# Kernel optimization log

Measured on AMD Instinct MI355X. Metric: run time of the kernel, lower is better.

## Reference

```python
import jax, jax.numpy as jnp
import numpy as np

L, D = 1024, 256
NDIR, NL = 6, 2
H, P, N, K = 8, 64, 32, 4          # nheads, headdim, d_state, d_conv
DI = 2 * D                          # d_inner = expand * d_model
DIN = 2 * DI + 2 * N + H            # in_proj output width (z, xBC, dt)
CONV_DIM = DI + 2 * N               # channels going through depthwise conv
ORDERS = [(0, 1, 2), (0, 2, 1), (1, 0, 2), (1, 2, 0), (2, 0, 1), (2, 1, 0)]  # XYT,XTY,YXT,YTX,TXY,TYX


def setup_inputs() -> dict:
    ks = jax.random.split(jax.random.key(0), 12)
    s = 0.02
    f32 = jnp.float32
    return {
        "vectors": jax.random.normal(ks[0], (L, D), f32),
        "event_coords": jax.random.randint(ks[1], (L, 4), 0, 64, jnp.int32),
        "ln_g": jnp.ones((NDIR, NL, D), f32),
        "ln_b": jnp.zeros((NDIR, NL, D), f32),
        "Win": jax.random.normal(ks[2], (NDIR, NL, D, DIN), f32) * s,
        "conv_w": jax.random.normal(ks[3], (NDIR, NL, CONV_DIM, K), f32) * s,
        "conv_b": jnp.zeros((NDIR, NL, CONV_DIM), f32),
        "dt_bias": jax.random.normal(ks[4], (NDIR, NL, H), f32) * 0.5,
        "A_log": jnp.log(jax.random.uniform(ks[5], (NDIR, NL, H), f32, 1.0, 16.0)),
        "Dp": jnp.ones((NDIR, NL, H), f32),
        "rms_g": jnp.ones((NDIR, NL, DI), f32),
        "Wout": jax.random.normal(ks[6], (NDIR, NL, DI, D), f32) * s,
        "fuse_ln_g": jnp.ones((NDIR * D,), f32),
        "fuse_ln_b": jnp.zeros((NDIR * D,), f32),
        "fuse_W": jax.random.normal(ks[7], (NDIR * D, D), f32) * s,
        "fuse_b": jnp.zeros((D,), f32),
    }


def _layernorm(x, g, b, eps=1e-5):
    mu = jnp.mean(x, -1, keepdims=True)
    var = jnp.mean((x - mu) ** 2, -1, keepdims=True)
    return (x - mu) * jax.lax.rsqrt(var + eps) * g + b


def _causal_dwconv(x, w, b):
    # x: [Bt,L,C]; w: [C,K]. Torch depthwise conv1d with padding K-1, truncated to L.
    k = w.shape[1]
    Lx = x.shape[1]
    xp = jnp.pad(x, ((0, 0), (k - 1, 0), (0, 0)))
    return sum(xp[:, j:j + Lx, :] * w[:, j] for j in range(k)) + b


def _mamba2(x, Win, conv_w, conv_b, dt_bias, A_log, Dp, rms_g, Wout):
    # x: [Bt,L,D] -> [Bt,L,D]. Mamba2 with ngroups=1, rmsnorm gating, no proj biases.
    Bt, Lx, _ = x.shape
    zxbcdt = x @ Win
    z = zxbcdt[..., :DI]
    xBC = zxbcdt[..., DI:DI + CONV_DIM]
    dt = jax.nn.softplus(zxbcdt[..., -H:] + dt_bias)              # [Bt,L,H]
    xBC = jax.nn.silu(_causal_dwconv(xBC, conv_w, conv_b))
    xs = xBC[..., :DI].reshape(Bt, Lx, H, P)                      # [Bt,L,H,P]
    Bm = xBC[..., DI:DI + N]                                      # [Bt,L,N]
    Cm = xBC[..., DI + N:]                                        # [Bt,L,N]
    dA = jnp.exp(dt * (-jnp.exp(A_log)))                          # [Bt,L,H]
    dBx = jnp.einsum('blh,bln,blhp->blhpn', dt, Bm, xs)

    def step(h, inp):
        dA_t, dBx_t, C_t = inp
        h = dA_t[:, :, None, None] * h + dBx_t                    # [Bt,H,P,N]
        return h, jnp.einsum('bhpn,bn->bhp', h, C_t)

    h0 = jnp.zeros((Bt, H, P, N), x.dtype)
    _, ys = jax.lax.scan(step, h0, (dA.transpose(1, 0, 2),
                                    dBx.transpose(1, 0, 2, 3, 4),
                                    Cm.transpose(1, 0, 2)))
    y = ys.transpose(1, 0, 2, 3) + Dp[:, None] * xs               # [Bt,L,H,P]
    u = y.reshape(Bt, Lx, DI) * jax.nn.silu(z)                    # gated RMSNorm
    u = u * jax.lax.rsqrt(jnp.mean(u * u, -1, keepdims=True) + 1e-5) * rms_g
    return u @ Wout


def _forward(vectors, event_coords, ln_g, ln_b, Win, conv_w, conv_b, dt_bias,
             A_log, Dp, rms_g, Wout, fuse_ln_g, fuse_ln_b, fuse_W, fuse_b):
    v = vectors[None]                                             # [1,L,D]
    outs = []
    for i, axes in enumerate(ORDERS):
        idx = jnp.lexsort(tuple(event_coords[:, a] for a in reversed(axes)))
        x = v[:, idx, :]
        for l in range(NL):
            x = x + _mamba2(_layernorm(x, ln_g[i, l], ln_b[i, l]),
                            Win[i, l], conv_w[i, l], conv_b[i, l], dt_bias[i, l],
                            A_log[i, l], Dp[i, l], rms_g[i, l], Wout[i, l])
        outs.append(x[:, jnp.argsort(idx), :])                    # scatter back
    md = jnp.concatenate(outs, -1)                                # [1,L,6D]
    f = _layernorm(md, fuse_ln_g, fuse_ln_b) @ fuse_W + fuse_b
    return jax.nn.gelu(f, approximate=False)[0]                   # [L,D]


def reference(vectors, event_coords, ln_g, ln_b, Win, conv_w, conv_b, dt_bias,
              A_log, Dp, rms_g, Wout, fuse_ln_g, fuse_ln_b, fuse_W, fuse_b):
    return _forward(vectors, event_coords, ln_g, ln_b, Win, conv_w, conv_b, dt_bias,
                    A_log, Dp, rms_g, Wout, fuse_ln_g, fuse_ln_b, fuse_W, fuse_b)
```

## Files before the change

kernel.cpp:

```cpp
#include <hip/hip_runtime.h>
#include <hip/hip_bf16.h>
#include <cstddef>

#define LL 1024
#define DD0 256
#define NDIR 6
#define NL 2
#define HH 8
#define PP 64
#define NN 32
#define KK 4
#define DI 512
#define DIN 1096
#define CONV_DIM 576

#define QC 32
#define NC 32
#define NCSH 5

__constant__ int c_ord[6][3] = {{0,1,2},{0,2,1},{1,0,2},{1,2,0},{2,0,1},{2,1,0}};

typedef __attribute__((ext_vector_type(8))) short bf16x8;
typedef __attribute__((ext_vector_type(4))) float f32x4;

__device__ inline float blockReduceSum256(float v) {
    __shared__ float sred[4];
#pragma unroll
    for (int off = 1; off < 64; off <<= 1) v += __shfl_xor(v, off);
    int lane = threadIdx.x & 63, w = threadIdx.x >> 6;
    __syncthreads();
    if (lane == 0) sred[w] = v;
    __syncthreads();
    return sred[0] + sred[1] + sred[2] + sred[3];
}

__device__ inline float siluf(float x) { return x / (1.f + expf(-x)); }

__device__ inline unsigned short bf16_rn(float x) {
    unsigned u = __float_as_uint(x);
    unsigned r = (u + 0x7fffu + ((u >> 16) & 1u)) >> 16;
    return (unsigned short)r;
}
__device__ inline float bf16_to_f(unsigned short h) {
    return __uint_as_float(((unsigned)h) << 16);
}

__global__ __launch_bounds__(1024)
void sort_kernel(const int* __restrict__ coords, int* __restrict__ perm, int* __restrict__ rank) {
    int d = blockIdx.x;
    int i = threadIdx.x;
    __shared__ unsigned keys[LL];
    int a0 = c_ord[d][0], a1 = c_ord[d][1], a2 = c_ord[d][2];
    unsigned c0 = (unsigned)coords[i*4 + a0];
    unsigned c1 = (unsigned)coords[i*4 + a1];
    unsigned c2 = (unsigned)coords[i*4 + a2];
    unsigned key = (c0 << 22) | (c1 << 16) | (c2 << 10) | (unsigned)i;
    keys[i] = key;
    __syncthreads();
    int r = 0;
    for (int j = 0; j < LL; ++j) r += (keys[j] < key) ? 1 : 0;
    perm[d*LL + r] = i;
    rank[d*LL + i] = r;
}

__global__ __launch_bounds__(256)
void gather_ln(const float* __restrict__ vectors, const int* __restrict__ perm,
               float* __restrict__ x, unsigned short* __restrict__ Yh,
               unsigned short* __restrict__ Yl,
               const float* __restrict__ g, const float* __restrict__ b) {
    int t = blockIdx.x, d = blockIdx.y, c = threadIdx.x;
    int src = perm[d*LL + t];
    float xv = vectors[(size_t)src*DD0 + c];
    x[((size_t)d*LL + t)*DD0 + c] = xv;
    float s = blockReduceSum256(xv);
    float s2 = blockReduceSum256(xv*xv);
    float mu = s / DD0;
    float var = s2 / DD0 - mu*mu;
    float inv = rsqrtf(var + 1e-5f);
    const float* gr = g + (size_t)d*NL*DD0;
    const float* br = b + (size_t)d*NL*DD0;
    float yv = (xv - mu) * inv * gr[c] + br[c];
    unsigned short h = bf16_rn(yv);
    Yh[((size_t)d*LL + t)*DD0 + c] = h;
    Yl[((size_t)d*LL + t)*DD0 + c] = bf16_rn(yv - bf16_to_f(h));
}

__global__ __launch_bounds__(256)
void ln_split(const float* __restrict__ X, unsigned short* __restrict__ Yh,
              unsigned short* __restrict__ Yl,
              const float* __restrict__ g, const float* __restrict__ b,
              int dd, int rowsPerDir, int gstride) {
    int t = blockIdx.x, d = blockIdx.y;
    const float* xr = X + ((size_t)d*rowsPerDir + t)*dd;
    unsigned short* yh = Yh + ((size_t)d*rowsPerDir + t)*dd;
    unsigned short* yl = Yl + ((size_t)d*rowsPerDir + t)*dd;
    const float* gr = g + (size_t)d*gstride;
    const float* br = b + (size_t)d*gstride;
    float v[6];
    float s = 0.f, s2 = 0.f;
    int cnt = 0;
    for (int c = threadIdx.x; c < dd; c += 256) {
        float xv = xr[c];
        v[cnt++] = xv;
        s += xv; s2 += xv*xv;
    }
    float tot = blockReduceSum256(s);
    float tot2 = blockReduceSum256(s2);
    float mu = tot / dd;
    float var = tot2 / dd - mu*mu;
    float inv = rsqrtf(var + 1e-5f);
    cnt = 0;
    for (int c = threadIdx.x; c < dd; c += 256) {
        float yv = (v[cnt++] - mu) * inv * gr[c] + br[c];
        unsigned short h = bf16_rn(yv);
        yh[c] = h;
        yl[c] = bf16_rn(yv - bf16_to_f(h));
    }
}

__global__ __launch_bounds__(256)
void ln_concat(const float* __restrict__ x, const int* __restrict__ rank,
               unsigned short* __restrict__ Yh, unsigned short* __restrict__ Yl,
               const float* __restrict__ g, const float* __restrict__ b) {
    int t = blockIdx.x, tid = threadIdx.x;
    float v[NDIR];
    float s = 0.f, s2 = 0.f;
#pragma unroll
    for (int d = 0; d < NDIR; ++d) {
        int r = rank[d*LL + t];
        float xv = x[((size_t)d*LL + r)*DD0 + tid];
        v[d] = xv;
        s += xv; s2 += xv*xv;
    }
    float tot = blockReduceSum256(s);
    float tot2 = blockReduceSum256(s2);
    const int dd = NDIR*DD0;
    float mu = tot / dd;
    float var = tot2 / dd - mu*mu;
    float inv = rsqrtf(var + 1e-5f);
#pragma unroll
    for (int d = 0; d < NDIR; ++d) {
        int c = d*DD0 + tid;
        float yv = (v[d] - mu) * inv * g[c] + b[c];
        unsigned short h = bf16_rn(yv);
        Yh[(size_t)t*dd + c] = h;
        Yl[(size_t)t*dd + c] = bf16_rn(yv - bf16_to_f(h));
    }
}

__global__ __launch_bounds__(256)
void tsplit_kernel(const float* __restrict__ W, unsigned short* __restrict__ Th,
                   unsigned short* __restrict__ Tl, int Kd, int Nd) {
    __shared__ float tile[32][33];
    int j0 = blockIdx.x * 32;
    int i0 = blockIdx.y * 32;
    int c = threadIdx.x & 31, r8 = threadIdx.x >> 5;
    const float* Wz = W + (size_t)blockIdx.z * Kd * Nd;
    unsigned short* Thz = Th + (size_t)blockIdx.z * Nd * Kd;
    unsigned short* Tlz = Tl + (size_t)blockIdx.z * Nd * Kd;
#pragma unroll
    for (int s = 0; s < 4; ++s) {
        int i = i0 + r8 + s*8;
        tile[r8 + s*8][c] = (i < Kd && (j0 + c) < Nd) ? Wz[(size_t)i*Nd + j0 + c] : 0.f;
    }
    __syncthreads();
#pragma unroll
    for (int s = 0; s < 4; ++s) {
        int j = j0 + r8 + s*8;
        int i = i0 + c;
        if (j < Nd && i < Kd) {
            float xv = tile[c][r8 + s*8];
            unsigned short h = bf16_rn(xv);
            Thz[(size_t)j*Kd + i] = h;
            Tlz[(size_t)j*Kd + i] = bf16_rn(xv - bf16_to_f(h));
        }
    }
}

template<int MODE, int BM>
__global__ __launch_bounds__(256)
void mfma_gemm(const unsigned short* __restrict__ Ahg, const unsigned short* __restrict__ Alg,
               const unsigned short* __restrict__ Bhg, const unsigned short* __restrict__ Blg,
               float* __restrict__ Cg, int N, int K,
               size_t sA, size_t sB, size_t sC, const float* __restrict__ bias) {
    constexpr int MF = BM / 32;
    __shared__ unsigned short AhS[2][BM][40];
    __shared__ unsigned short AlS[2][BM][40];
    __shared__ unsigned short BhS[2][64][40];
    __shared__ unsigned short BlS[2][64][40];
    const unsigned short* Azh = Ahg + (size_t)blockIdx.z * sA;
    const unsigned short* Azl = Alg + (size_t)blockIdx.z * sA;
    const unsigned short* Bzh = Bhg + (size_t)blockIdx.z * sB;
    const unsigned short* Bzl = Blg + (size_t)blockIdx.z * sB;
    float* Cz = Cg + (size_t)blockIdx.z * sC;
    int row0 = blockIdx.y * BM;
    int col0 = blockIdx.x * 64;
    int tid = threadIdx.x;
    int lane = tid & 63, wid = tid >> 6;
    int mbase = (wid >> 1) * (BM/2), nbase = (wid & 1) * 32;
    int lr = lane & 15, lk = (lane >> 4) * 8;

    int ar0 = tid >> 2;
    int ar1 = 64 + (tid >> 2);
    int ac  = (tid & 3) * 8;
    int brow = tid >> 2;
    int bc8 = (tid & 3) * 8;
    bool bvalid = (col0 + brow) < N;
    const uint4 z4 = {0u,0u,0u,0u};

    f32x4 acc[MF][2];
#pragma unroll
    for (int m = 0; m < MF; ++m)
#pragma unroll
        for (int n = 0; n < 2; ++n) acc[m][n] = (f32x4){0.f, 0.f, 0.f, 0.f};

    uint4 s0a0, s0a1, s0l0, s0l1, s0bh, s0bl;
    uint4 s1a0, s1a1, s1l0, s1l1, s1bh, s1bl;

#define LOAD_TILE(Ra0,Ra1,Rl0,Rl1,Rbh,Rbl,kt) do {                          \
        size_t ka = (size_t)(kt) * 32;                                       \
        size_t g0 = (size_t)(row0 + ar0)*K + ka + ac;                        \
        Ra0 = *(const uint4*)(Azh + g0);                                     \
        Rl0 = *(const uint4*)(Azl + g0);                                     \
        if (BM == 128) {                                                     \
            size_t g1 = (size_t)(row0 + ar1)*K + ka + ac;                    \
            Ra1 = *(const uint4*)(Azh + g1);                                 \
            Rl1 = *(const uint4*)(Azl + g1);                                 \
        }                                                                    \
        if (bvalid) {                                                        \
            size_t gb = (size_t)(col0 + brow)*K + ka + bc8;                  \
            Rbh = *(const uint4*)(Bzh + gb);                                 \
            Rbl = *(const uint4*)(Bzl + gb);                                 \
        } else { Rbh = z4; Rbl = z4; }                                       \
    } while (0)

#define WRITE_TILE(buf,Ra0,Ra1,Rl0,Rl1,Rbh,Rbl) do {                         \
        *(uint4*)&AhS[buf][ar0][ac] = Ra0;                                   \
        *(uint4*)&AlS[buf][ar0][ac] = Rl0;                                   \
        if (BM == 128) {                                                     \
            *(uint4*)&AhS[buf][ar1 & (BM-1)][ac] = Ra1;                      \
            *(uint4*)&AlS[buf][ar1 & (BM-1)][ac] = Rl1;                      \
        }                                                                    \
        *(uint4*)&BhS[buf][brow][bc8] = Rbh;                                 \
        *(uint4*)&BlS[buf][brow][bc8] = Rbl;                                 \
    } while (0)

#define COMPUTE(buf) do {                                                    \
        bf16x8 afh[MF], afl[MF], bfh[2], bfl[2];                             \
        _Pragma("unroll")                                                    \
        for (int mf = 0; mf < MF; ++mf) {                                    \
            afh[mf] = *(const bf16x8*)&AhS[buf][mbase + mf*16 + lr][lk];     \
            afl[mf] = *(const bf16x8*)&AlS[buf][mbase + mf*16 + lr][lk];     \
        }                                                                    \
        _Pragma("unroll")                                                    \
        for (int nf = 0; nf < 2; ++nf) {                                     \
            bfh[nf] = *(const bf16x8*)&BhS[buf][nbase + nf*16 + lr][lk];     \
            bfl[nf] = *(const bf16x8*)&BlS[buf][nbase + nf*16 + lr][lk];     \
        }                                                                    \
        _Pragma("unroll")                                                    \
        for (int mf = 0; mf < MF; ++mf)                                      \
            _Pragma("unroll")                                                \
            for (int nf = 0; nf < 2; ++nf) {                                 \
                acc[mf][nf] = __builtin_amdgcn_mfma_f32_16x16x32_bf16(afh[mf], bfh[nf], acc[mf][nf], 0, 0, 0); \
                acc[mf][nf] = __builtin_amdgcn_mfma_f32_16x16x32_bf16(afh[mf], bfl[nf], acc[mf][nf], 0, 0, 0); \
                acc[mf][nf] = __builtin_amdgcn_mfma_f32_16x16x32_bf16(afl[mf], bfh[nf], acc[mf][nf], 0, 0, 0); \
            }                                                                \
    } while (0)

    int nt = K >> 5;

    LOAD_TILE(s0a0, s0a1, s0l0, s0l1, s0bh, s0bl, 0);
    LOAD_TILE(s1a0, s1a1, s1l0, s1l1, s1bh, s1bl, 1);
    WRITE_TILE(0, s0a0, s0a1, s0l0, s0l1, s0bh, s0bl);
    __syncthreads();

    for (int t = 0; t < nt; t += 2) {
        if (t + 2 < nt) LOAD_TILE(s0a0, s0a1, s0l0, s0l1, s0bh, s0bl, t + 2);
        COMPUTE(0);
        WRITE_TILE(1, s1a0, s1a1, s1l0, s1l1, s1bh, s1bl);
        __syncthreads();
        if (t + 3 < nt) LOAD_TILE(s1a0, s1a1, s1l0, s1l1, s1bh, s1bl, t + 3);
        COMPUTE(1);
        if (t + 2 < nt) WRITE_TILE(0, s0a0, s0a1, s0l0, s0l1, s0bh, s0bl);
        __syncthreads();
    }

#undef LOAD_TILE
#undef WRITE_TILE
#undef COMPUTE

    int crb = (lane >> 4) * 4;
    int cco = lane & 15;
#pragma unroll
    for (int mf = 0; mf < MF; ++mf) {
#pragma unroll
        for (int nf = 0; nf < 2; ++nf) {
            int col = col0 + nbase + nf*16 + cco;
            if (col < N) {
#pragma unroll
                for (int r = 0; r < 4; ++r) {
                    int row = row0 + mbase + mf*16 + crb + r;
                    size_t o = (size_t)row*N + col;
                    float vv = acc[mf][nf][r];
                    if (MODE == 0) Cz[o] = vv;
                    else if (MODE == 1) Cz[o] += vv;
                    else {
                        vv += bias[col];
                        Cz[o] = 0.5f * vv * (1.f + erff(vv * 0.70710678118654752f));
                    }
                }
            }
        }
    }
}

__global__ __launch_bounds__(256)
void conv_scan1(const float* __restrict__ zx, const float* __restrict__ conv_w,
                const float* __restrict__ conv_b, const float* __restrict__ dt_bias,
                const float* __restrict__ A_log, const float* __restrict__ Dp,
                float* __restrict__ ys, float* __restrict__ Cbuf,
                float* __restrict__ cstate, float* __restrict__ cumdec, int layer) {
    int bid = blockIdx.x;
    int c = bid & (NC - 1);
    int hd = bid >> NCSH;
    int d = hd >> 3, h = hd & 7;
    int tid = threadIdx.x;
    int t0 = c * QC;

    __shared__ float sxc[QC][132];
    __shared__ float sdt[QC];
    __shared__ float sdA[QC];

    const float* Z = zx + (size_t)d*LL*DIN;

    {
        int col = tid & 127;
        int half = tid >> 7;
        int tstart = t0 + half*16;
        int realc = (col < 64) ? (h*PP + col) : ((col < 96) ? (DI + (col-64)) : (DI + NN + (col-96)));
        int zxcol = DI + realc;
        const float* wr = conv_w + ((size_t)(d*NL + layer)*CONV_DIM + realc)*KK;
        float w0 = wr[0], w1 = wr[1], w2 = wr[2], w3 = wr[3];
        float bias = conv_b[(size_t)(d*NL + layer)*CONV_DIM + realc];
        float z0 = (tstart-3 >= 0) ? Z[(size_t)(tstart-3)*DIN + zxcol] : 0.f;
        float z1 = (tstart-2 >= 0) ? Z[(size_t)(tstart-2)*DIN + zxcol] : 0.f;
        float z2 = (tstart-1 >= 0) ? Z[(size_t)(tstart-1)*DIN + zxcol] : 0.f;
#pragma unroll
        for (int tt = 0; tt < 16; ++tt) {
            int t = tstart + tt;
            float z3 = Z[(size_t)t*DIN + zxcol];
            float acc = bias;
            acc = fmaf(z0, w0, acc);
            acc = fmaf(z1, w1, acc);
            acc = fmaf(z2, w2, acc);
            acc = fmaf(z3, w3, acc);
            sxc[half*16 + tt][col] = siluf(acc);
            z0 = z1; z1 = z2; z2 = z3;
        }
    }
    if (tid < QC) {
        int t = t0 + tid;
        float v = Z[(size_t)t*DIN + (DIN - HH) + h] + dt_bias[(d*NL + layer)*HH + h];
        float sp = (v > 20.f) ? v : log1pf(expf(v));
        sdt[tid] = sp;
        sdA[tid] = expf(-expf(A_log[(d*NL + layer)*HH + h]) * sp);
    }
    __syncthreads();

    int p = tid >> 2, g = tid & 3, n0 = g << 3;
    float dpv = Dp[(d*NL + layer)*HH + h];
    float* ysd = ys + (size_t)d*LL*DI + h*PP + p;
    float* cdd = cumdec + (size_t)d*LL*HH + h;
    float* Cbd = Cbuf + (size_t)d*LL*NN;

    float hs[8];
#pragma unroll
    for (int j = 0; j < 8; ++j) hs[j] = 0.f;
    float cum = 1.f;

    for (int tt = 0; tt < QC; ++tt) {
        float dtv = sdt[tt], dAv = sdA[tt];
        float xv = sxc[tt][p];
        float dtx = dtv * xv;
        float4 b0 = *(const float4*)&sxc[tt][64 + n0];
        float4 b1 = *(const float4*)&sxc[tt][64 + n0 + 4];
        float4 c0 = *(const float4*)&sxc[tt][96 + n0];
        float4 c1 = *(const float4*)&sxc[tt][96 + n0 + 4];
        float B[8] = {b0.x,b0.y,b0.z,b0.w,b1.x,b1.y,b1.z,b1.w};
        float Cv[8] = {c0.x,c0.y,c0.z,c0.w,c1.x,c1.y,c1.z,c1.w};
        float acc = 0.f;
#pragma unroll
        for (int j = 0; j < 8; ++j) {
            hs[j] = fmaf(dAv, hs[j], dtx * B[j]);
            acc = fmaf(hs[j], Cv[j], acc);
        }
        acc += __shfl_xor(acc, 1);
        acc += __shfl_xor(acc, 2);
        int t = t0 + tt;
        if (g == 0) ysd[(size_t)t*DI] = acc + dpv * xv;
        else if (g == 2 && h == 0 && p < NN) Cbd[(size_t)t*NN + p] = sxc[tt][96 + p];
        cum *= dAv;
        if (tid == 0) cdd[(size_t)t*HH] = cum;
    }

    float* cs = cstate + (((size_t)(d*NC + c)*HH + h)*PP + p)*NN + n0;
    float4 s0 = {hs[0], hs[1], hs[2], hs[3]};
    float4 s1 = {hs[4], hs[5], hs[6], hs[7]};
    *(float4*)cs = s0;
    *(float4*)(cs + 4) = s1;
}

__global__ __launch_bounds__(256)
void scan_pass2(float* __restrict__ cstate, const float* __restrict__ cumdec) {
    int hd = blockIdx.x;
    int d = hd >> 3, h = hd & 7;
    int tid = threadIdx.x;
    int p = tid >> 2, g = tid & 3, n0 = g << 3;
    float carry[8];
#pragma unroll
    for (int j = 0; j < 8; ++j) carry[j] = 0.f;
    for (int c = 0; c < NC; ++c) {
        float* cs = cstate + (((size_t)(d*NC + c)*HH + h)*PP + p)*NN + n0;
        float4 s0 = *(const float4*)cs;
        float4 s1 = *(const float4*)(cs + 4);
        float4 w0 = {carry[0], carry[1], carry[2], carry[3]};
        float4 w1 = {carry[4], carry[5], carry[6], carry[7]};
        *(float4*)cs = w0;
        *(float4*)(cs + 4) = w1;
        float dec = cumdec[((size_t)d*LL + (c*QC + QC - 1))*HH + h];
        float s[8] = {s0.x,s0.y,s0.z,s0.w,s1.x,s1.y,s1.z,s1.w};
#pragma unroll
        for (int j = 0; j < 8; ++j) carry[j] = fmaf(dec, carry[j], s[j]);
    }
}

__global__ __launch_bounds__(256)
void scan_pass3(const float* __restrict__ Cbuf, const float* __restrict__ cumdec,
                const float* __restrict__ cstate, float* __restrict__ ys) {
    int bid = blockIdx.x;
    int c = bid & (NC - 1);
    if (c == 0) return;
    int hd = bid >> NCSH;
    int d = hd >> 3, h = hd & 7;
    int tid = threadIdx.x;
    int p = tid >> 2, g = tid & 3, n0 = g << 3;
    int t0 = c * QC;

    __shared__ float scd[QC];
    if (tid < QC) scd[tid] = cumdec[((size_t)d*LL + t0 + tid)*HH + h];

    const float* cs = cstate + (((size_t)(d*NC + c)*HH + h)*PP + p)*NN + n0;
    float4 h0 = *(const float4*)cs;
    float4 h1 = *(const float4*)(cs + 4);
    float hi[8] = {h0.x,h0.y,h0.z,h0.w,h1.x,h1.y,h1.z,h1.w};
    __syncthreads();

    const float* Cbd = Cbuf + (size_t)d*LL*NN;
    float* ysd = ys + (size_t)d*LL*DI + h*PP + p;

    for (int tt = 0; tt < QC; ++tt) {
        int t = t0 + tt;
        const float* row = Cbd + (size_t)t*NN;
        float4 c0 = *(const float4*)(row + n0);
        float4 c1 = *(const float4*)(row + n0 + 4);
        float Cv[8] = {c0.x,c0.y,c0.z,c0.w,c1.x,c1.y,c1.z,c1.w};
        float acc = 0.f;
#pragma unroll
        for (int j = 0; j < 8; ++j) acc = fmaf(hi[j], Cv[j], acc);
        acc += __shfl_xor(acc, 1);
        acc += __shfl_xor(acc, 2);
        if (g == 0) ysd[(size_t)t*DI] += scd[tt] * acc;
    }
}

__global__ __launch_bounds__(256)
void gate_rms(const float* __restrict__ ys, const float* __restrict__ zx,
              const float* __restrict__ rms_g, unsigned short* __restrict__ uh,
              unsigned short* __restrict__ ul, int layer) {
    int t = blockIdx.x, d = blockIdx.y;
    const float* ysr = ys + ((size_t)d*LL + t)*DI;
    const float* zr = zx + ((size_t)d*LL + t)*DIN;
    const float* rg = rms_g + (size_t)(d*NL + layer)*DI;
    unsigned short* uhr = uh + ((size_t)d*LL + t)*DI;
    unsigned short* ulr = ul + ((size_t)d*LL + t)*DI;
    float vals[2];
    float ss = 0.f;
#pragma unroll
    for (int i = 0; i < 2; ++i) {
        int c = threadIdx.x + i*256;
        float yv = ysr[c];
        float zv = zr[c];
        float uv = yv * siluf(zv);
        vals[i] = uv;
        ss += uv * uv;
    }
    float tot = blockReduceSum256(ss);
    float scale = rsqrtf(tot / DI + 1e-5f);
#pragma unroll
    for (int i = 0; i < 2; ++i) {
        int c = threadIdx.x + i*256;
        float uv = vals[i] * scale * rg[c];
        unsigned short h = bf16_rn(uv);
        uhr[c] = h;
        ulr[c] = bf16_rn(uv - bf16_to_f(h));
    }
}

extern "C" void kernel_launch(void* const* d_in, const int* in_sizes, int n_in,
                              void* d_out, int out_size, void* d_ws, size_t ws_size,
                              hipStream_t stream) {
    const float* vectors   = (const float*)d_in[0];
    const int*   coords    = (const int*)d_in[1];
    const float* ln_g      = (const float*)d_in[2];
    const float* ln_b      = (const float*)d_in[3];
    const float* Win       = (const float*)d_in[4];
    const float* conv_w    = (const float*)d_in[5];
    const float* conv_b    = (const float*)d_in[6];
    const float* dt_bias   = (const float*)d_in[7];
    const float* A_log     = (const float*)d_in[8];
    const float* Dp        = (const float*)d_in[9];
    const float* rms_g     = (const float*)d_in[10];
    const float* Wout      = (const float*)d_in[11];
    const float* fuse_ln_g = (const float*)d_in[12];
    const float* fuse_ln_b = (const float*)d_in[13];
    const float* fuse_W    = (const float*)d_in[14];
    const float* fuse_b    = (const float*)d_in[15];
    float* out = (float*)d_out;

    char* ws = (char*)d_ws;
    size_t off = 0;
    auto alloc = [&](size_t bytes) -> void* {
        void* p = ws + off;
        off += (bytes + 255) & ~(size_t)255;
        return p;
    };
    int* perm  = (int*)alloc((size_t)NDIR*LL*4);
    int* rank  = (int*)alloc((size_t)NDIR*LL*4);
    float* x   = (float*)alloc((size_t)NDIR*LL*DD0*4);
    unsigned short* xnh = (unsigned short*)alloc((size_t)NDIR*LL*DD0*2);
    unsigned short* xnl = (unsigned short*)alloc((size_t)NDIR*LL*DD0*2);
    float* zx  = (float*)alloc((size_t)NDIR*LL*DIN*4);
    float* Cbuf= (float*)alloc((size_t)NDIR*LL*NN*4);
    float* ysb = (float*)alloc((size_t)NDIR*LL*DI*4);
    unsigned short* uh = (unsigned short*)alloc((size_t)NDIR*LL*DI*2);
    unsigned short* ul = (unsigned short*)alloc((size_t)NDIR*LL*DI*2);
    float* cstate = (float*)alloc((size_t)NDIR*NC*HH*PP*NN*4);
    float* cumdec = (float*)alloc((size_t)NDIR*LL*HH*4);
    unsigned short* WinTh  = (unsigned short*)alloc((size_t)NDIR*NL*DIN*DD0*2);
    unsigned short* WinTl  = (unsigned short*)alloc((size_t)NDIR*NL*DIN*DD0*2);
    unsigned short* WoutTh = (unsigned short*)alloc((size_t)NDIR*NL*DD0*DI*2);
    unsigned short* WoutTl = (unsigned short*)alloc((size_t)NDIR*NL*DD0*DI*2);
    unsigned short* fWTh   = (unsigned short*)alloc((size_t)DD0*(NDIR*DD0)*2);
    unsigned short* fWTl   = (unsigned short*)alloc((size_t)DD0*(NDIR*DD0)*2);
    unsigned short* mdnh = uh;
    unsigned short* mdnl = ul;
    (void)ws_size;

    sort_kernel<<<NDIR, 1024, 0, stream>>>(coords, perm, rank);

    tsplit_kernel<<<dim3((DIN+31)/32, DD0/32, NDIR*NL), 256, 0, stream>>>(Win, WinTh, WinTl, DD0, DIN);
    tsplit_kernel<<<dim3(DD0/32, DI/32, NDIR*NL), 256, 0, stream>>>(Wout, WoutTh, WoutTl, DI, DD0);
    tsplit_kernel<<<dim3(DD0/32, (NDIR*DD0)/32, 1), 256, 0, stream>>>(fuse_W, fWTh, fWTl, NDIR*DD0, DD0);

    for (int l = 0; l < NL; ++l) {
        if (l == 0)
            gather_ln<<<dim3(LL, NDIR), 256, 0, stream>>>(vectors, perm, x, xnh, xnl, ln_g, ln_b);
        else
            ln_split<<<dim3(LL, NDIR), 256, 0, stream>>>(x, xnh, xnl, ln_g + l*DD0, ln_b + l*DD0,
                                                         DD0, LL, NL*DD0);
        mfma_gemm<0,64><<<dim3((DIN+63)/64, LL/64, NDIR), 256, 0, stream>>>(
            xnh, xnl, WinTh + (size_t)l*DIN*DD0, WinTl + (size_t)l*DIN*DD0, zx,
            DIN, DD0, (size_t)LL*DD0, (size_t)NL*DIN*DD0, (size_t)LL*DIN, nullptr);
        conv_scan1<<<NDIR*HH*NC, 256, 0, stream>>>(zx, conv_w, conv_b, dt_bias, A_log, Dp,
                                                   ysb, Cbuf, cstate, cumdec, l);
        scan_pass2<<<NDIR*HH, 256, 0, stream>>>(cstate, cumdec);
        scan_pass3<<<NDIR*HH*NC, 256, 0, stream>>>(Cbuf, cumdec, cstate, ysb);
        gate_rms<<<dim3(LL, NDIR), 256, 0, stream>>>(ysb, zx, rms_g, uh, ul, l);
        mfma_gemm<1,64><<<dim3(DD0/64, LL/64, NDIR), 256, 0, stream>>>(
            uh, ul, WoutTh + (size_t)l*DD0*DI, WoutTl + (size_t)l*DD0*DI, x,
            DD0, DI, (size_t)LL*DI, (size_t)NL*DD0*DI, (size_t)LL*DD0, nullptr);
    }

    ln_concat<<<LL, 256, 0, stream>>>(x, rank, mdnh, mdnl, fuse_ln_g, fuse_ln_b);
    mfma_gemm<2,64><<<dim3(DD0/64, LL/64, 1), 256, 0, stream>>>(
        mdnh, mdnl, fWTh, fWTl, out, DD0, NDIR*DD0, 0, 0, 0, fuse_b);
}
```

Baseline: 300.5 us.

## Load MFMA fragments directly from global memory, dropping LDS staging in GEMM

The split-bf16 GEMM kernel no longer stages A and B tiles through shared memory. Each lane loads its MFMA operand fragments straight from global memory into registers, using a two-stage register double buffer, and all __syncthreads barriers are gone. This removes LDS write/read traffic and barrier stalls. In exchange, each fragment is loaded redundantly by several waves, which relies on L1/L2 caching, and the per-lane 16-byte row-strided loads coalesce less well.

After: 698.8 us. 133% more time.

```diff
diff --git a/kernel.cpp b/kernel.cpp
--- a/kernel.cpp
+++ b/kernel.cpp
@@ -177,122 +177,90 @@
     }
 }
 
-template<int MODE, int BM>
+__device__ inline void mfma3(f32x4& acc, uint4 ah, uint4 al, uint4 bh, uint4 bl) {
+    bf16x8 AH = __builtin_bit_cast(bf16x8, ah);
+    bf16x8 AL = __builtin_bit_cast(bf16x8, al);
+    bf16x8 BH = __builtin_bit_cast(bf16x8, bh);
+    bf16x8 BL = __builtin_bit_cast(bf16x8, bl);
+    acc = __builtin_amdgcn_mfma_f32_16x16x32_bf16(AH, BH, acc, 0, 0, 0);
+    acc = __builtin_amdgcn_mfma_f32_16x16x32_bf16(AH, BL, acc, 0, 0, 0);
+    acc = __builtin_amdgcn_mfma_f32_16x16x32_bf16(AL, BH, acc, 0, 0, 0);
+}
+
+template<int MODE>
 __global__ __launch_bounds__(256)
 void mfma_gemm(const unsigned short* __restrict__ Ahg, const unsigned short* __restrict__ Alg,
                const unsigned short* __restrict__ Bhg, const unsigned short* __restrict__ Blg,
                float* __restrict__ Cg, int N, int K,
                size_t sA, size_t sB, size_t sC, const float* __restrict__ bias) {
-    constexpr int MF = BM / 32;
-    __shared__ unsigned short AhS[2][BM][40];
-    __shared__ unsigned short AlS[2][BM][40];
-    __shared__ unsigned short BhS[2][64][40];
-    __shared__ unsigned short BlS[2][64][40];
     const unsigned short* Azh = Ahg + (size_t)blockIdx.z * sA;
     const unsigned short* Azl = Alg + (size_t)blockIdx.z * sA;
     const unsigned short* Bzh = Bhg + (size_t)blockIdx.z * sB;
     const unsigned short* Bzl = Blg + (size_t)blockIdx.z * sB;
     float* Cz = Cg + (size_t)blockIdx.z * sC;
-    int row0 = blockIdx.y * BM;
+    int row0 = blockIdx.y * 64;
     int col0 = blockIdx.x * 64;
     int tid = threadIdx.x;
     int lane = tid & 63, wid = tid >> 6;
-    int mbase = (wid >> 1) * (BM/2), nbase = (wid & 1) * 32;
+    int mbase = (wid >> 1) * 32, nbase = (wid & 1) * 32;
     int lr = lane & 15, lk = (lane >> 4) * 8;
 
-    int ar0 = tid >> 2;
-    int ar1 = 64 + (tid >> 2);
-    int ac  = (tid & 3) * 8;
-    int brow = tid >> 2;
-    int bc8 = (tid & 3) * 8;
-    bool bvalid = (col0 + brow) < N;
+    size_t arow0 = (size_t)(row0 + mbase + lr) * K;
+    size_t arow1 = (size_t)(row0 + mbase + 16 + lr) * K;
+    int bcol0 = col0 + nbase + lr;
+    int bcol1 = col0 + nbase + 16 + lr;
+    bool bok0 = bcol0 < N, bok1 = bcol1 < N;
+    size_t brow0 = (size_t)(bok0 ? bcol0 : 0) * K;
+    size_t brow1 = (size_t)(bok1 ? bcol1 : 0) * K;
     const uint4 z4 = {0u,0u,0u,0u};
 
-    f32x4 acc[MF][2];
-#pragma unroll
-    for (int m = 0; m < MF; ++m)
+    f32x4 acc[2][2];
+#pragma unroll
+    for (int m = 0; m < 2; ++m)
 #pragma unroll
         for (int n = 0; n < 2; ++n) acc[m][n] = (f32x4){0.f, 0.f, 0.f, 0.f};
 
-    uint4 s0a0, s0a1, s0l0, s0l1, s0bh, s0bl;
-    uint4 s1a0, s1a1, s1l0, s1l1, s1bh, s1bl;
-
-#define LOAD_TILE(Ra0,Ra1,Rl0,Rl1,Rbh,Rbl,kt) do {                          \
-        size_t ka = (size_t)(kt) * 32;                                       \
-        size_t g0 = (size_t)(row0 + ar0)*K + ka + ac;                        \
-        Ra0 = *(const uint4*)(Azh + g0);                                     \
-        Rl0 = *(const uint4*)(Azl + g0);                                     \
-        if (BM == 128) {                                                     \
-            size_t g1 = (size_t)(row0 + ar1)*K + ka + ac;                    \
-            Ra1 = *(const uint4*)(Azh + g1);                                 \
-            Rl1 = *(const uint4*)(Azl + g1);                                 \
-        }                                                                    \
-        if (bvalid) {                                                        \
-            size_t gb = (size_t)(col0 + brow)*K + ka + bc8;                  \
-            Rbh = *(const uint4*)(Bzh + gb);                                 \
-            Rbl = *(const uint4*)(Bzl + gb);                                 \
-        } else { Rbh = z4; Rbl = z4; }                                       \
+    uint4 s0a0h, s0a0l, s0a1h, s0a1l, s0b0h, s0b0l, s0b1h, s0b1l;
+    uint4 s1a0h, s1a0l, s1a1h, s1a1l, s1b0h, s1b0l, s1b1h, s1b1l;
+
+#define LOADF(A0H,A0L,A1H,A1L,B0H,B0L,B1H,B1L,kt) do {                       \
+        size_t ko = (size_t)(kt)*32 + lk;                                     \
+        A0H = *(const uint4*)(Azh + arow0 + ko);                              \
+        A0L = *(const uint4*)(Azl + arow0 + ko);                              \
+        A1H = *(const uint4*)(Azh + arow1 + ko);                              \
+        A1L = *(const uint4*)(Azl + arow1 + ko);                              \
+        B0H = bok0 ? *(const uint4*)(Bzh + brow0 + ko) : z4;                  \
+        B0L = bok0 ? *(const uint4*)(Bzl + brow0 + ko) : z4;                  \
+        B1H = bok1 ? *(const uint4*)(Bzh + brow1 + ko) : z4;                  \
+        B1L = bok1 ? *(const uint4*)(Bzl + brow1 + ko) : z4;                  \
     } while (0)
 
-#define WRITE_TILE(buf,Ra0,Ra1,Rl0,Rl1,Rbh,Rbl) do {                         \
-        *(uint4*)&AhS[buf][ar0][ac] = Ra0;                                   \
-        *(uint4*)&AlS[buf][ar0][ac] = Rl0;                                   \
-        if (BM == 128) {                                                     \
-            *(uint4*)&AhS[buf][ar1 & (BM-1)][ac] = Ra1;                      \
-            *(uint4*)&AlS[buf][ar1 & (BM-1)][ac] = Rl1;                      \
-        }                                                                    \
-        *(uint4*)&BhS[buf][brow][bc8] = Rbh;                                 \
-        *(uint4*)&BlS[buf][brow][bc8] = Rbl;                                 \
+#define COMPUTEF(A0H,A0L,A1H,A1L,B0H,B0L,B1H,B1L) do {                        \
+        mfma3(acc[0][0], A0H, A0L, B0H, B0L);                                 \
+        mfma3(acc[0][1], A0H, A0L, B1H, B1L);                                 \
+        mfma3(acc[1][0], A1H, A1L, B0H, B0L);                                 \
+        mfma3(acc[1][1], A1H, A1L, B1H, B1L);                                 \
     } while (0)
 
-#define COMPUTE(buf) do {                                                    \
-        bf16x8 afh[MF], afl[MF], bfh[2], bfl[2];                             \
-        _Pragma("unroll")                                                    \
-        for (int mf = 0; mf < MF; ++mf) {                                    \
-            afh[mf] = *(const bf16x8*)&AhS[buf][mbase + mf*16 + lr][lk];     \
-            afl[mf] = *(const bf16x8*)&AlS[buf][mbase + mf*16 + lr][lk];     \
-        }                                                                    \
-        _Pragma("unroll")                                                    \
-        for (int nf = 0; nf < 2; ++nf) {                                     \
-            bfh[nf] = *(const bf16x8*)&BhS[buf][nbase + nf*16 + lr][lk];     \
-            bfl[nf] = *(const bf16x8*)&BlS[buf][nbase + nf*16 + lr][lk];     \
-        }                                                                    \
-        _Pragma("unroll")                                                    \
-        for (int mf = 0; mf < MF; ++mf)                                      \
-            _Pragma("unroll")                                                \
-            for (int nf = 0; nf < 2; ++nf) {                                 \
-                acc[mf][nf] = __builtin_amdgcn_mfma_f32_16x16x32_bf16(afh[mf], bfh[nf], acc[mf][nf], 0, 0, 0); \
-                acc[mf][nf] = __builtin_amdgcn_mfma_f32_16x16x32_bf16(afh[mf], bfl[nf], acc[mf][nf], 0, 0, 0); \
-                acc[mf][nf] = __builtin_amdgcn_mfma_f32_16x16x32_bf16(afl[mf], bfh[nf], acc[mf][nf], 0, 0, 0); \
-            }                                                                \
-    } while (0)
-
     int nt = K >> 5;
 
-    LOAD_TILE(s0a0, s0a1, s0l0, s0l1, s0bh, s0bl, 0);
-    LOAD_TILE(s1a0, s1a1, s1l0, s1l1, s1bh, s1bl, 1);
-    WRITE_TILE(0, s0a0, s0a1, s0l0, s0l1, s0bh, s0bl);
-    __syncthreads();
+    LOADF(s0a0h,s0a0l,s0a1h,s0a1l,s0b0h,s0b0l,s0b1h,s0b1l, 0);
+    LOADF(s1a0h,s1a0l,s1a1h,s1a1l,s1b0h,s1b0l,s1b1h,s1b1l, 1);
 
     for (int t = 0; t < nt; t += 2) {
-        if (t + 2 < nt) LOAD_TILE(s0a0, s0a1, s0l0, s0l1, s0bh, s0bl, t + 2);
-        COMPUTE(0);
-        WRITE_TILE(1, s1a0, s1a1, s1l0, s1l1, s1bh, s1bl);
-        __syncthreads();
-        if (t + 3 < nt) LOAD_TILE(s1a0, s1a1, s1l0, s1l1, s1bh, s1bl, t + 3);
-        COMPUTE(1);
-        if (t + 2 < nt) WRITE_TILE(0, s0a0, s0a1, s0l0, s0l1, s0bh, s0bl);
-        __syncthreads();
-    }
-
-#undef LOAD_TILE
-#undef WRITE_TILE
-#undef COMPUTE
+        COMPUTEF(s0a0h,s0a0l,s0a1h,s0a1l,s0b0h,s0b0l,s0b1h,s0b1l);
+        if (t + 2 < nt) LOADF(s0a0h,s0a0l,s0a1h,s0a1l,s0b0h,s0b0l,s0b1h,s0b1l, t + 2);
+        COMPUTEF(s1a0h,s1a0l,s1a1h,s1a1l,s1b0h,s1b0l,s1b1h,s1b1l);
+        if (t + 3 < nt) LOADF(s1a0h,s1a0l,s1a1h,s1a1l,s1b0h,s1b0l,s1b1h,s1b1l, t + 3);
+    }
+
+#undef LOADF
+#undef COMPUTEF
 
     int crb = (lane >> 4) * 4;
     int cco = lane & 15;
 #pragma unroll
-    for (int mf = 0; mf < MF; ++mf) {
+    for (int mf = 0; mf < 2; ++mf) {
 #pragma unroll
         for (int nf = 0; nf < 2; ++nf) {
             int col = col0 + nbase + nf*16 + cco;
@@ -568,7 +536,7 @@
         else
             ln_split<<<dim3(LL, NDIR), 256, 0, stream>>>(x, xnh, xnl, ln_g + l*DD0, ln_b + l*DD0,
                                                          DD0, LL, NL*DD0);
-        mfma_gemm<0,64><<<dim3((DIN+63)/64, LL/64, NDIR), 256, 0, stream>>>(
+        mfma_gemm<0><<<dim3((DIN+63)/64, LL/64, NDIR), 256, 0, stream>>>(
             xnh, xnl, WinTh + (size_t)l*DIN*DD0, WinTl + (size_t)l*DIN*DD0, zx,
             DIN, DD0, (size_t)LL*DD0, (size_t)NL*DIN*DD0, (size_t)LL*DIN, nullptr);
         conv_scan1<<<NDIR*HH*NC, 256, 0, stream>>>(zx, conv_w, conv_b, dt_bias, A_log, Dp,
@@ -576,12 +544,12 @@
         scan_pass2<<<NDIR*HH, 256, 0, stream>>>(cstate, cumdec);
         scan_pass3<<<NDIR*HH*NC, 256, 0, stream>>>(Cbuf, cumdec, cstate, ysb);
         gate_rms<<<dim3(LL, NDIR), 256, 0, stream>>>(ysb, zx, rms_g, uh, ul, l);
-        mfma_gemm<1,64><<<dim3(DD0/64, LL/64, NDIR), 256, 0, stream>>>(
+        mfma_gemm<1><<<dim3(DD0/64, LL/64, NDIR), 256, 0, stream>>>(
             uh, ul, WoutTh + (size_t)l*DD0*DI, WoutTl + (size_t)l*DD0*DI, x,
             DD0, DI, (size_t)LL*DI, (size_t)NL*DD0*DI, (size_t)LL*DD0, nullptr);
     }
 
     ln_concat<<<LL, 256, 0, stream>>>(x, rank, mdnh, mdnl, fuse_ln_g, fuse_ln_b);
-    mfma_gemm<2,64><<<dim3(DD0/64, LL/64, 1), 256, 0, stream>>>(
+    mfma_gemm<2><<<dim3(DD0/64, LL/64, 1), 256, 0, stream>>>(
         mdnh, mdnl, fWTh, fWTl, out, DD0, NDIR*DD0, 0, 0, 0, fuse_b);
 }
```

## Split-K the final fusion GEMM and vectorize gate_rms loads and stores

Applied to the files above, without the earlier changes.

The final fusion GEMM (K=1536) previously ran on only 64 blocks. It is now split four ways along K into a partial buffer, and a separate reduce kernel sums the partials, adds the bias and applies GELU. This raises parallelism for that tail GEMM at the cost of an extra launch and extra global traffic. gate_rms also switches to float2 loads and packed 32-bit bf16 stores to cut memory instructions.

Result: faster. 286.3 us (-4.7%).

```diff
diff --git a/kernel.cpp b/kernel.cpp
--- a/kernel.cpp
+++ b/kernel.cpp
@@ -182,16 +182,17 @@
 void mfma_gemm(const unsigned short* __restrict__ Ahg, const unsigned short* __restrict__ Alg,
                const unsigned short* __restrict__ Bhg, const unsigned short* __restrict__ Blg,
                float* __restrict__ Cg, int N, int K,
-               size_t sA, size_t sB, size_t sC, const float* __restrict__ bias) {
+               size_t sA, size_t sB, size_t sC, const float* __restrict__ bias,
+               int ksplit) {
     constexpr int MF = BM / 32;
     __shared__ unsigned short AhS[2][BM][40];
     __shared__ unsigned short AlS[2][BM][40];
     __shared__ unsigned short BhS[2][64][40];
     __shared__ unsigned short BlS[2][64][40];
-    const unsigned short* Azh = Ahg + (size_t)blockIdx.z * sA;
-    const unsigned short* Azl = Alg + (size_t)blockIdx.z * sA;
-    const unsigned short* Bzh = Bhg + (size_t)blockIdx.z * sB;
-    const unsigned short* Bzl = Blg + (size_t)blockIdx.z * sB;
+    const unsigned short* Azh = Ahg + (MODE == 3 ? 0 : (size_t)blockIdx.z * sA);
+    const unsigned short* Azl = Alg + (MODE == 3 ? 0 : (size_t)blockIdx.z * sA);
+    const unsigned short* Bzh = Bhg + (MODE == 3 ? 0 : (size_t)blockIdx.z * sB);
+    const unsigned short* Bzl = Blg + (MODE == 3 ? 0 : (size_t)blockIdx.z * sB);
     float* Cz = Cg + (size_t)blockIdx.z * sC;
     int row0 = blockIdx.y * BM;
     int col0 = blockIdx.x * 64;
@@ -267,19 +268,21 @@
             }                                                                \
     } while (0)
 
-    int nt = K >> 5;
-
-    LOAD_TILE(s0a0, s0a1, s0l0, s0l1, s0bh, s0bl, 0);
-    LOAD_TILE(s1a0, s1a1, s1l0, s1l1, s1bh, s1bl, 1);
+    int nt, kt0;
+    if (MODE == 3) { nt = ksplit; kt0 = (int)blockIdx.z * ksplit; }
+    else           { nt = K >> 5; kt0 = 0; }
+
+    LOAD_TILE(s0a0, s0a1, s0l0, s0l1, s0bh, s0bl, kt0 + 0);
+    LOAD_TILE(s1a0, s1a1, s1l0, s1l1, s1bh, s1bl, kt0 + 1);
     WRITE_TILE(0, s0a0, s0a1, s0l0, s0l1, s0bh, s0bl);
     __syncthreads();
 
     for (int t = 0; t < nt; t += 2) {
-        if (t + 2 < nt) LOAD_TILE(s0a0, s0a1, s0l0, s0l1, s0bh, s0bl, t + 2);
+        if (t + 2 < nt) LOAD_TILE(s0a0, s0a1, s0l0, s0l1, s0bh, s0bl, kt0 + t + 2);
         COMPUTE(0);
         WRITE_TILE(1, s1a0, s1a1, s1l0, s1l1, s1bh, s1bl);
         __syncthreads();
-        if (t + 3 < nt) LOAD_TILE(s1a0, s1a1, s1l0, s1l1, s1bh, s1bl, t + 3);
+        if (t + 3 < nt) LOAD_TILE(s1a0, s1a1, s1l0, s1l1, s1bh, s1bl, kt0 + t + 3);
         COMPUTE(1);
         if (t + 2 < nt) WRITE_TILE(0, s0a0, s0a1, s0l0, s0l1, s0bh, s0bl);
         __syncthreads();
@@ -302,7 +305,7 @@
                     int row = row0 + mbase + mf*16 + crb + r;
                     size_t o = (size_t)row*N + col;
                     float vv = acc[mf][nf][r];
-                    if (MODE == 0) Cz[o] = vv;
+                    if (MODE == 0 || MODE == 3) Cz[o] = vv;
                     else if (MODE == 1) Cz[o] += vv;
                     else {
                         vv += bias[col];
@@ -312,6 +315,16 @@
             }
         }
     }
+}
+
+__global__ __launch_bounds__(256)
+void reduce_gelu(const float* __restrict__ pbuf, const float* __restrict__ bias,
+                 float* __restrict__ out) {
+    int t = blockIdx.x, c = threadIdx.x;
+    size_t o = (size_t)t*DD0 + c;
+    const size_t st = (size_t)LL*DD0;
+    float v = pbuf[o] + pbuf[o + st] + pbuf[o + 2*st] + pbuf[o + 3*st] + bias[c];
+    out[o] = 0.5f * v * (1.f + erff(v * 0.70710678118654752f));
 }
 
 __global__ __launch_bounds__(256)
@@ -483,27 +496,21 @@
     const float* rg = rms_g + (size_t)(d*NL + layer)*DI;
     unsigned short* uhr = uh + ((size_t)d*LL + t)*DI;
     unsigned short* ulr = ul + ((size_t)d*LL + t)*DI;
-    float vals[2];
-    float ss = 0.f;
-#pragma unroll
-    for (int i = 0; i < 2; ++i) {
-        int c = threadIdx.x + i*256;
-        float yv = ysr[c];
-        float zv = zr[c];
-        float uv = yv * siluf(zv);
-        vals[i] = uv;
-        ss += uv * uv;
-    }
+    int c2 = threadIdx.x * 2;
+    float2 yv = *(const float2*)(ysr + c2);
+    float2 zv = *(const float2*)(zr + c2);
+    float u0 = yv.x * siluf(zv.x);
+    float u1 = yv.y * siluf(zv.y);
+    float ss = u0*u0 + u1*u1;
     float tot = blockReduceSum256(ss);
     float scale = rsqrtf(tot / DI + 1e-5f);
-#pragma unroll
-    for (int i = 0; i < 2; ++i) {
-        int c = threadIdx.x + i*256;
-        float uv = vals[i] * scale * rg[c];
-        unsigned short h = bf16_rn(uv);
-        uhr[c] = h;
-        ulr[c] = bf16_rn(uv - bf16_to_f(h));
-    }
+    float2 rgv = *(const float2*)(rg + c2);
+    float o0 = u0 * scale * rgv.x;
+    float o1 = u1 * scale * rgv.y;
+    unsigned short h0 = bf16_rn(o0), h1 = bf16_rn(o1);
+    unsigned short l0 = bf16_rn(o0 - bf16_to_f(h0)), l1 = bf16_rn(o1 - bf16_to_f(h1));
+    *(unsigned*)(uhr + c2) = (unsigned)h0 | ((unsigned)h1 << 16);
+    *(unsigned*)(ulr + c2) = (unsigned)l0 | ((unsigned)l1 << 16);
 }
 
 extern "C" void kernel_launch(void* const* d_in, const int* in_sizes, int n_in,
@@ -546,6 +553,7 @@
     unsigned short* ul = (unsigned short*)alloc((size_t)NDIR*LL*DI*2);
     float* cstate = (float*)alloc((size_t)NDIR*NC*HH*PP*NN*4);
     float* cumdec = (float*)alloc((size_t)NDIR*LL*HH*4);
+    float* pbuf  = (float*)alloc((size_t)4*LL*DD0*4);
     unsigned short* WinTh  = (unsigned short*)alloc((size_t)NDIR*NL*DIN*DD0*2);
     unsigned short* WinTl  = (unsigned short*)alloc((size_t)NDIR*NL*DIN*DD0*2);
     unsigned short* WoutTh = (unsigned short*)alloc((size_t)NDIR*NL*DD0*DI*2);
@@ -570,7 +578,7 @@
                                                          DD0, LL, NL*DD0);
         mfma_gemm<0,64><<<dim3((DIN+63)/64, LL/64, NDIR), 256, 0, stream>>>(
             xnh, xnl, WinTh + (size_t)l*DIN*DD0, WinTl + (size_t)l*DIN*DD0, zx,
-            DIN, DD0, (size_t)LL*DD0, (size_t)NL*DIN*DD0, (size_t)LL*DIN, nullptr);
+            DIN, DD0, (size_t)LL*DD0, (size_t)NL*DIN*DD0, (size_t)LL*DIN, nullptr, 0);
         conv_scan1<<<NDIR*HH*NC, 256, 0, stream>>>(zx, conv_w, conv_b, dt_bias, A_log, Dp,
                                                    ysb, Cbuf, cstate, cumdec, l);
         scan_pass2<<<NDIR*HH, 256, 0, stream>>>(cstate, cumdec);
@@ -578,10 +586,11 @@
         gate_rms<<<dim3(LL, NDIR), 256, 0, stream>>>(ysb, zx, rms_g, uh, ul, l);
         mfma_gemm<1,64><<<dim3(DD0/64, LL/64, NDIR), 256, 0, stream>>>(
             uh, ul, WoutTh + (size_t)l*DD0*DI, WoutTl + (size_t)l*DD0*DI, x,
-            DD0, DI, (size_t)LL*DI, (size_t)NL*DD0*DI, (size_t)LL*DD0, nullptr);
+            DD0, DI, (size_t)LL*DI, (size_t)NL*DD0*DI, (size_t)LL*DD0, nullptr, 0);
     }
 
     ln_concat<<<LL, 256, 0, stream>>>(x, rank, mdnh, mdnl, fuse_ln_g, fuse_ln_b);
-    mfma_gemm<2,64><<<dim3(DD0/64, LL/64, 1), 256, 0, stream>>>(
-        mdnh, mdnl, fWTh, fWTl, out, DD0, NDIR*DD0, 0, 0, 0, fuse_b);
-}
+    mfma_gemm<3,64><<<dim3(DD0/64, LL/64, 4), 256, 0, stream>>>(
+        mdnh, mdnl, fWTh, fWTl, pbuf, DD0, NDIR*DD0, 0, 0, (size_t)LL*DD0, nullptr, 12);
+    reduce_gelu<<<LL, 256, 0, stream>>>(pbuf, fuse_b, out);
+}
```
